# Kernel tuning notes

Hardware: AMD Instinct MI355X
Metric: run time of the kernel (lower is better)

The kernel has to match this reference:

```python
import jax, jax.numpy as jnp
import numpy as np
import math

NUM_HEADS = 32
NUM_KV_HEADS = 8
HEAD_DIM = 128
ROPE_THETA = 10000.0


def _rope_cos_sin(position_ids, head_dim, dtype):
    # inv_freq: [head_dim/2]
    inv_freq = 1.0 / (ROPE_THETA ** (jnp.arange(0, head_dim, 2, dtype=jnp.float32) / head_dim))
    # freqs: [B, S, head_dim/2]
    freqs = position_ids.astype(jnp.float32)[:, :, None] * inv_freq[None, None, :]
    emb = jnp.concatenate([freqs, freqs], axis=-1)  # [B, S, head_dim]
    return jnp.cos(emb).astype(dtype), jnp.sin(emb).astype(dtype)


def _rotate_half(x):
    h = x.shape[-1] // 2
    return jnp.concatenate([-x[..., h:], x[..., :h]], axis=-1)


def setup_inputs() -> dict:
    key = jax.random.key(0)
    ks = jax.random.split(key, 5)
    B, S, H = 1, 2048, 4096
    kv_dim = NUM_KV_HEADS * HEAD_DIM
    return {
        "hidden_states": jax.random.normal(ks[0], (B, S, H), dtype=jnp.float32),
        "position_ids": jnp.arange(S, dtype=jnp.int64 if jax.config.jax_enable_x64 else jnp.int32)[None, :].repeat(B, axis=0),
        "Wq": jax.random.normal(ks[1], (H, H), dtype=jnp.float32) * 0.02,
        "Wk": jax.random.normal(ks[2], (kv_dim, H), dtype=jnp.float32) * 0.02,
        "Wv": jax.random.normal(ks[3], (kv_dim, H), dtype=jnp.float32) * 0.02,
        "Wo": jax.random.normal(ks[4], (H, H), dtype=jnp.float32) * 0.02,
    }


def reference(hidden_states, position_ids, Wq, Wk, Wv, Wo):
    B, S, H = hidden_states.shape
    groups = NUM_HEADS // NUM_KV_HEADS

    # QKV projections (nn.Linear: x @ W.T, no bias)
    q = (hidden_states @ Wq.T).reshape(B, S, NUM_HEADS, HEAD_DIM).transpose(0, 2, 1, 3)
    k = (hidden_states @ Wk.T).reshape(B, S, NUM_KV_HEADS, HEAD_DIM).transpose(0, 2, 1, 3)
    v = (hidden_states @ Wv.T).reshape(B, S, NUM_KV_HEADS, HEAD_DIM).transpose(0, 2, 1, 3)

    # RoPE
    cos, sin = _rope_cos_sin(position_ids, HEAD_DIM, q.dtype)
    cos = cos[:, None, :, :]  # [B,1,S,hd]
    sin = sin[:, None, :, :]
    q = q * cos + _rotate_half(q) * sin
    k = k * cos + _rotate_half(k) * sin

    # repeat_kv: expand KV heads to match Q heads
    k = jnp.repeat(k, groups, axis=1)  # [B, NUM_HEADS, S, hd]
    v = jnp.repeat(v, groups, axis=1)

    # scores + causal mask + fp32 softmax
    scores = jnp.einsum("bhqd,bhkd->bhqk", q, k) / math.sqrt(HEAD_DIM)
    causal = jnp.tril(jnp.ones((S, S), dtype=bool))
    scores = jnp.where(causal[None, None, :, :], scores, jnp.finfo(jnp.float32).min)
    attn = jax.nn.softmax(scores.astype(jnp.float32), axis=-1).astype(q.dtype)

    # attention output + output projection
    out = jnp.einsum("bhqk,bhkd->bhqd", attn, v)
    out = out.transpose(0, 2, 1, 3).reshape(B, S, H)
    return out @ Wo.T
```

## Files before the change

### kernel.cpp

```cpp
#include <hip/hip_runtime.h>
#include <stdint.h>


typedef __attribute__((ext_vector_type(8))) __bf16 bf16x8;
typedef __attribute__((ext_vector_type(4))) float floatx4;

#define S_LEN 2048
#define HID   4096
#define NH    32
#define NKV   8
#define HD    128

__device__ __forceinline__ unsigned short f2bf(float f) {
  union { float f; uint32_t u; } v; v.f = f;
  return (unsigned short)((v.u + 0x7fffu + ((v.u >> 16) & 1u)) >> 16);
}

__device__ __forceinline__ void gload_lds16(const unsigned short* g, unsigned short* l) {
  __builtin_amdgcn_global_load_lds(
      (const __attribute__((address_space(1))) void*)g,
      (__attribute__((address_space(3))) void*)l,
      16, 0, 0);
}

__global__ void cast_bf16_kernel(const float* __restrict__ in,
                                 unsigned short* __restrict__ out, int n4) {
  int i = blockIdx.x * blockDim.x + threadIdx.x;
  if (i >= n4) return;
  float4 f = ((const float4*)in)[i];
  ushort4 o = make_ushort4(f2bf(f.x), f2bf(f.y), f2bf(f.z), f2bf(f.w));
  ((ushort4*)out)[i] = o;
}

#define BM 128
#define BN 128
#define BK 32

__global__ __launch_bounds__(256) void gemm_bt_kernel(
    const unsigned short* __restrict__ A,
    const unsigned short* __restrict__ B,
    float* __restrict__ C, int M, int N, int K) {
  __shared__ unsigned short As[BM * BK];
  __shared__ unsigned short Bs[BN * BK];
  const int m0 = blockIdx.y * BM;
  const int n0 = blockIdx.x * BN;
  const int tid = threadIdx.x;
  const int lane = tid & 63;
  const int l15 = lane & 15;
  const int quad = lane >> 4;
  const int w = tid >> 6;
  const int wm = (w >> 1) * 64;
  const int wn = (w & 1) * 64;

  floatx4 acc[4][4];
#pragma unroll
  for (int i = 0; i < 4; i++)
#pragma unroll
    for (int j = 0; j < 4; j++) acc[i][j] = (floatx4){0.f, 0.f, 0.f, 0.f};

  const int c0 = tid, c1 = tid + 256;
  const int r0 = c0 >> 2, o0 = (c0 & 3) * 8;
  const int r1 = c1 >> 2, o1 = (c1 & 3) * 8;

  for (int k0 = 0; k0 < K; k0 += BK) {
    __syncthreads();
    gload_lds16(A + (size_t)(m0 + r0) * K + k0 + o0, As + c0 * 8);
    gload_lds16(A + (size_t)(m0 + r1) * K + k0 + o1, As + c1 * 8);
    gload_lds16(B + (size_t)(n0 + r0) * K + k0 + o0, Bs + c0 * 8);
    gload_lds16(B + (size_t)(n0 + r1) * K + k0 + o1, Bs + c1 * 8);
    __syncthreads();

    bf16x8 a_frag[4], b_frag[4];
#pragma unroll
    for (int mt = 0; mt < 4; mt++)
      a_frag[mt] = *(const bf16x8*)&As[(wm + mt * 16 + l15) * BK + quad * 8];
#pragma unroll
    for (int nt = 0; nt < 4; nt++)
      b_frag[nt] = *(const bf16x8*)&Bs[(wn + nt * 16 + l15) * BK + quad * 8];
#pragma unroll
    for (int mt = 0; mt < 4; mt++)
#pragma unroll
      for (int nt = 0; nt < 4; nt++)
        acc[mt][nt] = __builtin_amdgcn_mfma_f32_16x16x32_bf16(
            a_frag[mt], b_frag[nt], acc[mt][nt], 0, 0, 0);
  }

#pragma unroll
  for (int mt = 0; mt < 4; mt++) {
#pragma unroll
    for (int nt = 0; nt < 4; nt++) {
      const int row = m0 + wm + mt * 16 + quad * 4;
      const int col = n0 + wn + nt * 16 + l15;
#pragma unroll
      for (int r = 0; r < 4; r++)
        C[(size_t)(row + r) * N + col] = acc[mt][nt][r];
    }
  }
}

__global__ void rope_kernel(const float* __restrict__ Cqkv,
                            const int* __restrict__ pos_ids,
                            unsigned short* __restrict__ Qb,
                            unsigned short* __restrict__ Kb) {
  int t = blockIdx.x * blockDim.x + threadIdx.x;
  int j = t & 63;
  int s = t >> 6;
  int hh = blockIdx.y;
  float pos = (float)pos_ids[s];
  float ang = pos * exp2f(-0.20762050593045222f * (float)j);
  float c = cosf(ang), sn = sinf(ang);
  if (hh < NH) {
    const float* row = Cqkv + (size_t)s * 6144 + hh * HD;
    float x1 = row[j], x2 = row[j + 64];
    unsigned short* q = Qb + ((size_t)hh * S_LEN + s) * HD;
    q[j]      = f2bf(x1 * c - x2 * sn);
    q[j + 64] = f2bf(x2 * c + x1 * sn);
  } else {
    int kh = hh - NH;
    const float* row = Cqkv + (size_t)s * 6144 + HID + kh * HD;
    float x1 = row[j], x2 = row[j + 64];
    unsigned short* k = Kb + ((size_t)kh * S_LEN + s) * HD;
    k[j]      = f2bf(x1 * c - x2 * sn);
    k[j + 64] = f2bf(x2 * c + x1 * sn);
  }
}

__global__ void vtrans_kernel(const float* __restrict__ Cqkv,
                              unsigned short* __restrict__ Vt) {
  int t = blockIdx.x * blockDim.x + threadIdx.x;
  int s = t & (S_LEN - 1);
  int d = (t >> 11) & (HD - 1);
  int kh = t >> 18;
  Vt[((size_t)kh * HD + d) * S_LEN + s] =
      f2bf(Cqkv[(size_t)s * 6144 + (HID + NKV * HD) + kh * HD + d]);
}

__global__ __launch_bounds__(256) void flash_attn_kernel(
    const unsigned short* __restrict__ Qb, const unsigned short* __restrict__ Kb,
    const unsigned short* __restrict__ Vt, unsigned short* __restrict__ O) {
  __shared__ unsigned short Ks[64 * 128];
  __shared__ unsigned short Vs[128 * 64];
  __shared__ unsigned short Ps[4][2][16 * 72];
  const int qb = gridDim.x - 1 - blockIdx.x;
  const int q0 = qb * 128;
  const int h = blockIdx.y;
  const int kvh = h >> 2;
  const int tid = threadIdx.x;
  const int lane = tid & 63;
  const int w = tid >> 6;
  const int l15 = lane & 15;
  const int quad = lane >> 4;
  const int qlo = q0 + w * 32;

  const unsigned short* Qh = Qb + (size_t)h * S_LEN * HD;
  const unsigned short* Kh = Kb + (size_t)kvh * S_LEN * HD;
  const unsigned short* Vh = Vt + (size_t)kvh * HD * S_LEN;

  bf16x8 q_frag[2][4];
#pragma unroll
  for (int mf = 0; mf < 2; mf++)
#pragma unroll
    for (int kk = 0; kk < 4; kk++)
      q_frag[mf][kk] = *(const bf16x8*)&Qh[(size_t)(qlo + mf * 16 + l15) * HD + kk * 32 + quad * 8];

  bf16x8 ones_frag;
  {
    union { unsigned short u; __bf16 b; } ov;
    ov.u = (l15 == 0) ? 0x3F80 : 0;
#pragma unroll
    for (int j = 0; j < 8; j++) ones_frag[j] = ov.b;
  }

  floatx4 o_acc[2][8];
  floatx4 o_l[2];
#pragma unroll
  for (int mf = 0; mf < 2; mf++) {
#pragma unroll
    for (int i = 0; i < 8; i++) o_acc[mf][i] = (floatx4){0.f, 0.f, 0.f, 0.f};
    o_l[mf] = (floatx4){0.f, 0.f, 0.f, 0.f};
  }
  const float SC2 = 0.12751738f;

  const int nkt = q0 / 64 + 2;
  for (int kt = 0; kt < nkt; kt++) {
    const int kbase = kt * 64;
    __syncthreads();
#pragma unroll
    for (int it = 0; it < 4; it++) {
      int c = tid + it * 256;
      int kr = c >> 4, kj = (c & 15) ^ (kr & 15);
      gload_lds16(Kh + (size_t)(kbase + kr) * HD + kj * 8, Ks + c * 8);
      int vd = c >> 3, vj = (c & 7) ^ (vd & 7);
      gload_lds16(Vh + (size_t)vd * S_LEN + kbase + vj * 8, Vs + c * 8);
    }
    __syncthreads();

    if (kbase <= qlo + 31) {
      floatx4 s_acc[2][4];
#pragma unroll
      for (int mf = 0; mf < 2; mf++)
#pragma unroll
        for (int nt = 0; nt < 4; nt++) s_acc[mf][nt] = (floatx4){0.f, 0.f, 0.f, 0.f};
#pragma unroll
      for (int kk = 0; kk < 4; kk++)
#pragma unroll
        for (int nt = 0; nt < 4; nt++) {
          bf16x8 k_frag = *(const bf16x8*)&Ks[(nt * 16 + l15) * 128 + (((kk * 4 + quad) ^ l15) * 8)];
#pragma unroll
          for (int mf = 0; mf < 2; mf++)
            s_acc[mf][nt] = __builtin_amdgcn_mfma_f32_16x16x32_bf16(
                q_frag[mf][kk], k_frag, s_acc[mf][nt], 0, 0, 0);
        }

      const bool diag = (kbase + 63 > qlo);
      if (diag) {
#pragma unroll
        for (int mf = 0; mf < 2; mf++) {
#pragma unroll
          for (int nt = 0; nt < 4; nt++) {
            int kc = kbase + nt * 16 + l15;
            int qrow = qlo + mf * 16 + quad * 4;
#pragma unroll
            for (int r = 0; r < 4; r++) {
              float pv = exp2f(s_acc[mf][nt][r] * SC2);
              if (kc > qrow + r) pv = 0.f;
              Ps[w][mf][(quad * 4 + r) * 72 + nt * 16 + l15] = f2bf(pv);
            }
          }
        }
      } else {
#pragma unroll
        for (int mf = 0; mf < 2; mf++)
#pragma unroll
          for (int nt = 0; nt < 4; nt++)
#pragma unroll
            for (int r = 0; r < 4; r++)
              Ps[w][mf][(quad * 4 + r) * 72 + nt * 16 + l15] =
                  f2bf(exp2f(s_acc[mf][nt][r] * SC2));
      }

#pragma unroll
      for (int kk2 = 0; kk2 < 2; kk2++) {
        bf16x8 p_frag[2];
#pragma unroll
        for (int mf = 0; mf < 2; mf++)
          p_frag[mf] = *(const bf16x8*)&Ps[w][mf][l15 * 72 + kk2 * 32 + quad * 8];
#pragma unroll
        for (int dt = 0; dt < 8; dt++) {
          bf16x8 v_frag = *(const bf16x8*)&Vs[(dt * 16 + l15) * 64 + (((kk2 * 4 + quad) ^ (l15 & 7)) * 8)];
#pragma unroll
          for (int mf = 0; mf < 2; mf++)
            o_acc[mf][dt] = __builtin_amdgcn_mfma_f32_16x16x32_bf16(
                p_frag[mf], v_frag, o_acc[mf][dt], 0, 0, 0);
        }
#pragma unroll
        for (int mf = 0; mf < 2; mf++)
          o_l[mf] = __builtin_amdgcn_mfma_f32_16x16x32_bf16(
              p_frag[mf], ones_frag, o_l[mf], 0, 0, 0);
      }
    }
  }

#pragma unroll
  for (int mf = 0; mf < 2; mf++)
#pragma unroll
    for (int r = 0; r < 4; r++) {
      float lsum = __shfl(o_l[mf][r], lane & 48, 64);
      float inv = 1.f / lsum;
      int qr = qlo + mf * 16 + quad * 4 + r;
#pragma unroll
      for (int dt = 0; dt < 8; dt++)
        O[(size_t)qr * HID + h * HD + dt * 16 + l15] = f2bf(o_acc[mf][dt][r] * inv);
    }
}

extern "C" void kernel_launch(void* const* d_in, const int* in_sizes, int n_in,
                              void* d_out, int out_size, void* d_ws, size_t ws_size,
                              hipStream_t stream) {
  const float* hidden = (const float*)d_in[0];
  const int*   pos    = (const int*)d_in[1];
  const float* Wq     = (const float*)d_in[2];
  const float* Wk     = (const float*)d_in[3];
  const float* Wv     = (const float*)d_in[4];
  const float* Wo     = (const float*)d_in[5];

  char* ws = (char*)d_ws;
  size_t off = 0;
  unsigned short* h_b    = (unsigned short*)(ws + off); off += (size_t)S_LEN * HID * 2;
  unsigned short* Wqkv_b = (unsigned short*)(ws + off); off += (size_t)6144 * HID * 2;
  unsigned short* Wo_b   = (unsigned short*)(ws + off); off += (size_t)HID * HID * 2;
  float*          Cqkv   = (float*)(ws + off);          off += (size_t)S_LEN * 6144 * 4;
  unsigned short* Qb     = (unsigned short*)(ws + off); off += (size_t)NH * S_LEN * HD * 2;
  unsigned short* Kb     = (unsigned short*)(ws + off); off += (size_t)NKV * S_LEN * HD * 2;
  unsigned short* Vt     = (unsigned short*)(ws + off); off += (size_t)NKV * HD * S_LEN * 2;
  unsigned short* attn_b = (unsigned short*)Cqkv;

  cast_bf16_kernel<<<(S_LEN * HID / 4) / 256, 256, 0, stream>>>(hidden, h_b, S_LEN * HID / 4);
  cast_bf16_kernel<<<(HID * HID / 4) / 256, 256, 0, stream>>>(Wq, Wqkv_b, HID * HID / 4);
  cast_bf16_kernel<<<(1024 * HID / 4) / 256, 256, 0, stream>>>(Wk, Wqkv_b + (size_t)4096 * HID, 1024 * HID / 4);
  cast_bf16_kernel<<<(1024 * HID / 4) / 256, 256, 0, stream>>>(Wv, Wqkv_b + (size_t)5120 * HID, 1024 * HID / 4);
  cast_bf16_kernel<<<(HID * HID / 4) / 256, 256, 0, stream>>>(Wo, Wo_b, HID * HID / 4);

  gemm_bt_kernel<<<dim3(6144 / BN, S_LEN / BM), 256, 0, stream>>>(h_b, Wqkv_b, Cqkv, S_LEN, 6144, HID);

  rope_kernel<<<dim3(S_LEN * 64 / 256, NH + NKV), 256, 0, stream>>>(Cqkv, pos, Qb, Kb);
  vtrans_kernel<<<(NKV * HD * S_LEN) / 256, 256, 0, stream>>>(Cqkv, Vt);

  flash_attn_kernel<<<dim3(S_LEN / 128, NH), 256, 0, stream>>>(Qb, Kb, Vt, attn_b);

  gemm_bt_kernel<<<dim3(HID / BN, S_LEN / BM), 256, 0, stream>>>(attn_b, Wo_b, (float*)d_out, S_LEN, HID, HID);
}
```

Before: 643.7 us.

## Double-buffer K/V tiles in flash attention and swizzle the P scratch buffer

The attention kernel now prefetches the next K/V tile into a second LDS buffer while computing on the current one. This drops one of the two barriers per iteration, so global load latency can overlap with the MFMA work. The P staging buffer loses its row padding and uses an XOR swizzle to avoid bank conflicts, the masked and unmasked softmax branches are merged into one loop, and launch bounds request 2 blocks per CU. The cost is doubled K/V LDS use, and correctness relies on the barrier at the top of the loop also waiting for the async LDS loads to land.

```diff
diff --git a/kernel.cpp b/kernel.cpp
--- a/kernel.cpp
+++ b/kernel.cpp
@@ -135,12 +135,12 @@
       f2bf(Cqkv[(size_t)s * 6144 + (HID + NKV * HD) + kh * HD + d]);
 }
 
-__global__ __launch_bounds__(256) void flash_attn_kernel(
+__global__ __launch_bounds__(256, 2) void flash_attn_kernel(
     const unsigned short* __restrict__ Qb, const unsigned short* __restrict__ Kb,
     const unsigned short* __restrict__ Vt, unsigned short* __restrict__ O) {
-  __shared__ unsigned short Ks[64 * 128];
-  __shared__ unsigned short Vs[128 * 64];
-  __shared__ unsigned short Ps[4][2][16 * 72];
+  __shared__ unsigned short Ks[2][64 * 128];
+  __shared__ unsigned short Vs[2][128 * 64];
+  __shared__ unsigned short Ps[4][2][16 * 64];
   const int qb = gridDim.x - 1 - blockIdx.x;
   const int q0 = qb * 128;
   const int h = blockIdx.y;
@@ -156,6 +156,18 @@
   const unsigned short* Kh = Kb + (size_t)kvh * S_LEN * HD;
   const unsigned short* Vh = Vt + (size_t)kvh * HD * S_LEN;
 
+  const int kr_[4] = {(tid) >> 4, (tid + 256) >> 4, (tid + 512) >> 4, (tid + 768) >> 4};
+  const int nkt = q0 / 64 + 2;
+
+#pragma unroll
+  for (int it = 0; it < 4; it++) {
+    int c = tid + it * 256;
+    int kr = c >> 4, kj = (c & 15) ^ (kr & 15);
+    gload_lds16(Kh + (size_t)kr * HD + kj * 8, Ks[0] + c * 8);
+    int vd = c >> 3, vj = (c & 7) ^ (vd & 7);
+    gload_lds16(Vh + (size_t)vd * S_LEN + vj * 8, Vs[0] + c * 8);
+  }
+
   bf16x8 q_frag[2][4];
 #pragma unroll
   for (int mf = 0; mf < 2; mf++)
@@ -181,19 +193,22 @@
   }
   const float SC2 = 0.12751738f;
 
-  const int nkt = q0 / 64 + 2;
   for (int kt = 0; kt < nkt; kt++) {
     const int kbase = kt * 64;
+    const int buf = kt & 1;
     __syncthreads();
-#pragma unroll
-    for (int it = 0; it < 4; it++) {
-      int c = tid + it * 256;
-      int kr = c >> 4, kj = (c & 15) ^ (kr & 15);
-      gload_lds16(Kh + (size_t)(kbase + kr) * HD + kj * 8, Ks + c * 8);
-      int vd = c >> 3, vj = (c & 7) ^ (vd & 7);
-      gload_lds16(Vh + (size_t)vd * S_LEN + kbase + vj * 8, Vs + c * 8);
+
+    if (kt + 1 < nkt) {
+      const int kb2 = kbase + 64;
+#pragma unroll
+      for (int it = 0; it < 4; it++) {
+        int c = tid + it * 256;
+        int kr = c >> 4, kj = (c & 15) ^ (kr & 15);
+        gload_lds16(Kh + (size_t)(kb2 + kr) * HD + kj * 8, Ks[buf ^ 1] + c * 8);
+        int vd = c >> 3, vj = (c & 7) ^ (vd & 7);
+        gload_lds16(Vh + (size_t)vd * S_LEN + kb2 + vj * 8, Vs[buf ^ 1] + c * 8);
+      }
     }
-    __syncthreads();
 
     if (kbase <= qlo + 31) {
       floatx4 s_acc[2][4];
@@ -205,7 +220,7 @@
       for (int kk = 0; kk < 4; kk++)
 #pragma unroll
         for (int nt = 0; nt < 4; nt++) {
-          bf16x8 k_frag = *(const bf16x8*)&Ks[(nt * 16 + l15) * 128 + (((kk * 4 + quad) ^ l15) * 8)];
+          bf16x8 k_frag = *(const bf16x8*)&Ks[buf][(nt * 16 + l15) * 128 + (((kk * 4 + quad) ^ l15) * 8)];
 #pragma unroll
           for (int mf = 0; mf < 2; mf++)
             s_acc[mf][nt] = __builtin_amdgcn_mfma_f32_16x16x32_bf16(
@@ -213,30 +228,22 @@
         }
 
       const bool diag = (kbase + 63 > qlo);
-      if (diag) {
-#pragma unroll
-        for (int mf = 0; mf < 2; mf++) {
-#pragma unroll
-          for (int nt = 0; nt < 4; nt++) {
-            int kc = kbase + nt * 16 + l15;
-            int qrow = qlo + mf * 16 + quad * 4;
-#pragma unroll
-            for (int r = 0; r < 4; r++) {
-              float pv = exp2f(s_acc[mf][nt][r] * SC2);
-              if (kc > qrow + r) pv = 0.f;
-              Ps[w][mf][(quad * 4 + r) * 72 + nt * 16 + l15] = f2bf(pv);
-            }
+#pragma unroll
+      for (int mf = 0; mf < 2; mf++) {
+#pragma unroll
+        for (int nt = 0; nt < 4; nt++) {
+          int kc = kbase + nt * 16 + l15;
+          int qrow = qlo + mf * 16 + quad * 4;
+          int chunk2 = nt * 2 + (l15 >> 3);
+          int coff = l15 & 7;
+#pragma unroll
+          for (int r = 0; r < 4; r++) {
+            float pv = exp2f(s_acc[mf][nt][r] * SC2);
+            if (diag && kc > qrow + r) pv = 0.f;
+            int row = quad * 4 + r;
+            Ps[w][mf][row * 64 + ((chunk2 ^ (row & 7)) * 8) + coff] = f2bf(pv);
           }
         }
-      } else {
-#pragma unroll
-        for (int mf = 0; mf < 2; mf++)
-#pragma unroll
-          for (int nt = 0; nt < 4; nt++)
-#pragma unroll
-            for (int r = 0; r < 4; r++)
-              Ps[w][mf][(quad * 4 + r) * 72 + nt * 16 + l15] =
-                  f2bf(exp2f(s_acc[mf][nt][r] * SC2));
       }
 
 #pragma unroll
@@ -244,10 +251,10 @@
         bf16x8 p_frag[2];
 #pragma unroll
         for (int mf = 0; mf < 2; mf++)
-          p_frag[mf] = *(const bf16x8*)&Ps[w][mf][l15 * 72 + kk2 * 32 + quad * 8];
+          p_frag[mf] = *(const bf16x8*)&Ps[w][mf][l15 * 64 + (((kk2 * 4 + quad) ^ (l15 & 7)) * 8)];
 #pragma unroll
         for (int dt = 0; dt < 8; dt++) {
-          bf16x8 v_frag = *(const bf16x8*)&Vs[(dt * 16 + l15) * 64 + (((kk2 * 4 + quad) ^ (l15 & 7)) * 8)];
+          bf16x8 v_frag = *(const bf16x8*)&Vs[buf][(dt * 16 + l15) * 64 + (((kk2 * 4 + quad) ^ (l15 & 7)) * 8)];
 #pragma unroll
           for (int mf = 0; mf < 2; mf++)
             o_acc[mf][dt] = __builtin_amdgcn_mfma_f32_16x16x32_bf16(
```

New measurement: 590.9 us. 8.2% less time.
